# Performance work log

Measured on AMD Instinct MI355X. Metric: run time of the kernel, lower is better.

## Reference

```python
import jax, jax.numpy as jnp
import numpy as np

N = 1024        # hidden_size
M = 16000       # output_size (vocab)
T = 50          # encoder sequence length
NP = 50         # max_length (attention proj dim n_prime)


def setup_inputs() -> dict:
    key = jax.random.key(0)
    ks = jax.random.split(key, 24)
    f32 = jnp.float32
    def rnd(k, shape):
        return jax.random.normal(k, shape, dtype=f32) * 0.02
    inp = {
        'output': jax.random.normal(ks[0], (M, 1), dtype=f32),
        'hidden': jax.random.normal(ks[1], (N, 1), dtype=f32),
        'encoder_outputs': jax.random.normal(ks[2], (T, 2 * N), dtype=f32),
        # decoder GRU-like weights
        'W':  rnd(ks[3], (M, N)),
        'Wz': rnd(ks[4], (M, N)),
        'Wr': rnd(ks[5], (M, N)),
        'Wo': rnd(ks[6], (M, 2 * N)),
        'U':  rnd(ks[7], (N, N)),
        'Uz': rnd(ks[8], (N, N)),
        'Ur': rnd(ks[9], (N, N)),
        'Uo': rnd(ks[10], (4 * N, N)),
        'C':  rnd(ks[11], (2 * N, N)),
        'Cz': rnd(ks[12], (2 * N, N)),
        'Cr': rnd(ks[13], (2 * N, N)),
        'Co': rnd(ks[14], (4 * N, 2 * N)),
        'Vo': rnd(ks[15], (4 * N, M)),
        # attention weights
        'Va': rnd(ks[16], (NP, 1)),
        'Wa': rnd(ks[17], (NP, N)),
        'Ua': rnd(ks[18], (NP, 2 * N)),
    }
    return inp


def reference(output, hidden, encoder_outputs, W, Wz, Wr, Wo, U, Uz, Ur, Uo,
              C, Cz, Cr, Co, Vo, Va, Wa, Ua):
    y, s, h = output, hidden, encoder_outputs  # (M,1), (N,1), (T,2N)
    # --- Bahdanau attention (vectorized version of get_c's python loop) ---
    # e_i = exp(Va^T tanh(Wa@s + Ua@h_i)); then normalized -> softmax
    scores = jnp.tanh((Wa @ s).T + h @ Ua.T) @ Va          # (T,1)
    attn = jax.nn.softmax(scores[:, 0])                     # (T,)
    alpha = h * attn[:, None]                               # (T,2N) weighted enc outputs
    c = jnp.sum(alpha, axis=0)[:, None]                     # (2N,1) context
    # --- GRU-like decoder step (note: s_tilde uses sigmoid, per source) ---
    r = jax.nn.sigmoid(Wr.T @ y + Ur.T @ s + Cr.T @ c)      # (N,1)
    z = jax.nn.sigmoid(Wz.T @ y + Uz.T @ s + Cz.T @ c)      # (N,1)
    s_tilde = jax.nn.sigmoid(W.T @ y + U.T @ (r * s) + C.T @ c)
    s_new = (1.0 - z) * s + z * s_tilde                     # (N,1)
    # --- maxout output layer ---
    t_tilde = jax.nn.sigmoid(Uo @ s_new + Vo @ y + Co @ c)  # (4N,1)
    t = jnp.max(t_tilde.reshape(-1, 2, 1), axis=1)          # (2N,1) pairwise max
    logits = Wo @ t                                         # (M,1)
    log_sm = jax.nn.log_softmax(logits, axis=0)             # log(softmax(., dim=0))
    # dropout in the source is applied to a discarded value -> mathematical no-op
    return (log_sm, s_new, alpha)
```

## Files before the change

kernel.cpp:

```cpp
#include <hip/hip_runtime.h>
#include <math.h>

#define DEV_INLINE __device__ __forceinline__

DEV_INLINE float sigmoidf_(float x) { return 1.0f / (1.0f + expf(-x)); }

DEV_INLINE void colgemv_block(const float* __restrict__ A, const float* __restrict__ x,
                              float* __restrict__ out, int r0, int r1) {
    int c4 = threadIdx.x;
    const float4* A4 = (const float4*)A;
    float4 acc = make_float4(0.f, 0.f, 0.f, 0.f);
    for (int r = r0; r < r1; ++r) {
        float xv = x[r];
        float4 a = A4[(size_t)r * 256 + c4];
        acc.x = fmaf(xv, a.x, acc.x);
        acc.y = fmaf(xv, a.y, acc.y);
        acc.z = fmaf(xv, a.z, acc.z);
        acc.w = fmaf(xv, a.w, acc.w);
    }
    int c = c4 * 4;
    atomicAdd(out + c + 0, acc.x);
    atomicAdd(out + c + 1, acc.y);
    atomicAdd(out + c + 2, acc.z);
    atomicAdd(out + c + 3, acc.w);
}

DEV_INLINE float wave_dot(const float* __restrict__ row, const float* __restrict__ x,
                          int nv, int lane) {
    const float4* r4 = (const float4*)row;
    const float4* x4 = (const float4*)x;
    float acc = 0.f;
    for (int i = lane; i < nv; i += 64) {
        float4 a = r4[i], b = x4[i];
        acc = fmaf(a.x, b.x, fmaf(a.y, b.y, fmaf(a.z, b.z, fmaf(a.w, b.w, acc))));
    }
#pragma unroll
    for (int off = 32; off; off >>= 1) acc += __shfl_down(acc, off, 64);
    return acc;
}

__global__ void k_phaseA(const float* __restrict__ W, const float* __restrict__ Wz,
                         const float* __restrict__ Wr, const float* __restrict__ Uz,
                         const float* __restrict__ Ur, const float* __restrict__ Vo,
                         const float* __restrict__ Wa, const float* __restrict__ y,
                         const float* __restrict__ s, float* acc_r, float* acc_z,
                         float* acc_st, float* acc_t, float* ws50) {
    int b = blockIdx.x;
    if (b < 128) { colgemv_block(W, y, acc_st, b * 125, b * 125 + 125); return; }
    b -= 128;
    if (b < 128) { colgemv_block(Wz, y, acc_z, b * 125, b * 125 + 125); return; }
    b -= 128;
    if (b < 128) { colgemv_block(Wr, y, acc_r, b * 125, b * 125 + 125); return; }
    b -= 128;
    if (b < 8) { colgemv_block(Uz, s, acc_z, b * 128, b * 128 + 128); return; }
    b -= 8;
    if (b < 8) { colgemv_block(Ur, s, acc_r, b * 128, b * 128 + 128); return; }
    b -= 8;
    if (b < 1024) {
        int wid = (b * 256 + threadIdx.x) >> 6;
        int lane = threadIdx.x & 63;
        float v = wave_dot(Vo + (size_t)wid * 16000, y, 4000, lane);
        if (lane == 0) acc_t[wid] = v;
        return;
    }
    b -= 1024;
    {
        int wid = (b * 256 + threadIdx.x) >> 6;
        int lane = threadIdx.x & 63;
        if (wid < 50) {
            float v = wave_dot(Wa + wid * 1024, s, 256, lane);
            if (lane == 0) ws50[wid] = v;
        }
    }
}

__global__ void k_escore(const float* __restrict__ h, const float* __restrict__ Ua,
                         const float* __restrict__ ws50, float* __restrict__ em) {
    int wid = (blockIdx.x * blockDim.x + threadIdx.x) >> 6;
    int lane = threadIdx.x & 63;
    if (wid >= 2500) return;
    int i = wid / 50, j = wid - i * 50;
    float d = wave_dot(h + i * 2048, Ua + j * 2048, 512, lane);
    if (lane == 0) em[wid] = tanhf(ws50[j] + d);
}

__global__ void k_alpha_c(const float* __restrict__ h, const float* __restrict__ Va,
                          const float* __restrict__ em, float* __restrict__ cvec,
                          float* __restrict__ alpha_out) {
    __shared__ float attn_s[50];
    int tid = threadIdx.x;
    if (tid < 64) {
        float sc = -1e30f;
        if (tid < 50) {
            float t = 0.f;
            for (int j = 0; j < 50; ++j) t = fmaf(Va[j], em[tid * 50 + j], t);
            sc = t;
        }
        float m = sc;
#pragma unroll
        for (int off = 32; off; off >>= 1) m = fmaxf(m, __shfl_xor(m, off, 64));
        float e = (tid < 50) ? expf(sc - m) : 0.f;
        float ssum = e;
#pragma unroll
        for (int off = 32; off; off >>= 1) ssum += __shfl_xor(ssum, off, 64);
        if (tid < 50) attn_s[tid] = e / ssum;
    }
    __syncthreads();
    int g = blockIdx.x * 256 + tid;
    float csum = 0.f;
    for (int i = 0; i < 50; ++i) {
        float a = h[i * 2048 + g] * attn_s[i];
        alpha_out[i * 2048 + g] = a;
        csum += a;
    }
    cvec[g] = csum;
}

__global__ void k_phaseB(const float* __restrict__ C, const float* __restrict__ Cz,
                         const float* __restrict__ Cr, const float* __restrict__ cvec,
                         float* acc_st, float* acc_z, float* acc_r) {
    int b = blockIdx.x;
    if (b < 16) { colgemv_block(C, cvec, acc_st, b * 128, b * 128 + 128); return; }
    b -= 16;
    if (b < 16) { colgemv_block(Cz, cvec, acc_z, b * 128, b * 128 + 128); return; }
    b -= 16;
    colgemv_block(Cr, cvec, acc_r, b * 128, b * 128 + 128);
}

__global__ void k_rz(const float* __restrict__ acc_r, const float* __restrict__ acc_z,
                     const float* __restrict__ s, float* __restrict__ rs,
                     float* __restrict__ zbuf) {
    int n = blockIdx.x * 256 + threadIdx.x;
    float r = sigmoidf_(acc_r[n]);
    zbuf[n] = sigmoidf_(acc_z[n]);
    rs[n] = r * s[n];
}

__global__ void k_Ust(const float* __restrict__ U, const float* __restrict__ rs,
                      float* acc_st) {
    int b = blockIdx.x;
    colgemv_block(U, rs, acc_st, b * 128, b * 128 + 128);
}

__global__ void k_snew(const float* __restrict__ acc_st, const float* __restrict__ zbuf,
                       const float* __restrict__ s, float* __restrict__ snew,
                       float* __restrict__ out_snew) {
    int n = blockIdx.x * 256 + threadIdx.x;
    float st = sigmoidf_(acc_st[n]);
    float z = zbuf[n];
    float v = (1.f - z) * s[n] + z * st;
    snew[n] = v;
    out_snew[n] = v;
}

__global__ void k_uoco(const float* __restrict__ Uo, const float* __restrict__ Co,
                       const float* __restrict__ snew, const float* __restrict__ cvec,
                       float* __restrict__ acc_t) {
    int wid = (blockIdx.x * 256 + threadIdx.x) >> 6;
    int lane = threadIdx.x & 63;
    float d1 = wave_dot(Uo + (size_t)wid * 1024, snew, 256, lane);
    float d2 = wave_dot(Co + (size_t)wid * 2048, cvec, 512, lane);
    if (lane == 0) acc_t[wid] += d1 + d2;
}

__global__ void k_tmax(const float* __restrict__ acc_t, float* __restrict__ tvec) {
    int k = blockIdx.x * 256 + threadIdx.x;
    tvec[k] = fmaxf(sigmoidf_(acc_t[2 * k]), sigmoidf_(acc_t[2 * k + 1]));
}

__global__ void k_wo(const float* __restrict__ Wo, const float* __restrict__ tvec,
                     float* __restrict__ logits) {
    int wid = (blockIdx.x * 256 + threadIdx.x) >> 6;
    int lane = threadIdx.x & 63;
    float v = wave_dot(Wo + (size_t)wid * 2048, tvec, 512, lane);
    if (lane == 0) logits[wid] = v;
}

__global__ void k_logsm(float* __restrict__ out) {
    __shared__ float red[16];
    __shared__ float bval;
    int tid = threadIdx.x, lane = tid & 63, w = tid >> 6;
    float m = -1e30f;
    for (int i = tid; i < 16000; i += 1024) m = fmaxf(m, out[i]);
#pragma unroll
    for (int off = 32; off; off >>= 1) m = fmaxf(m, __shfl_xor(m, off, 64));
    if (lane == 0) red[w] = m;
    __syncthreads();
    if (tid == 0) {
        float mm = red[0];
        for (int i = 1; i < 16; ++i) mm = fmaxf(mm, red[i]);
        bval = mm;
    }
    __syncthreads();
    float M = bval;
    float sum = 0.f;
    for (int i = tid; i < 16000; i += 1024) sum += expf(out[i] - M);
#pragma unroll
    for (int off = 32; off; off >>= 1) sum += __shfl_xor(sum, off, 64);
    if (lane == 0) red[w] = sum;
    __syncthreads();
    if (tid == 0) {
        float ss = 0.f;
        for (int i = 0; i < 16; ++i) ss += red[i];
        bval = M + logf(ss);
    }
    __syncthreads();
    float lse = bval;
    for (int i = tid; i < 16000; i += 1024) out[i] -= lse;
}

extern "C" void kernel_launch(void* const* d_in, const int* in_sizes, int n_in,
                              void* d_out, int out_size, void* d_ws, size_t ws_size,
                              hipStream_t stream) {
    const float* y  = (const float*)d_in[0];
    const float* s  = (const float*)d_in[1];
    const float* h  = (const float*)d_in[2];
    const float* W  = (const float*)d_in[3];
    const float* Wz = (const float*)d_in[4];
    const float* Wr = (const float*)d_in[5];
    const float* Wo = (const float*)d_in[6];
    const float* U  = (const float*)d_in[7];
    const float* Uz = (const float*)d_in[8];
    const float* Ur = (const float*)d_in[9];
    const float* Uo = (const float*)d_in[10];
    const float* C  = (const float*)d_in[11];
    const float* Cz = (const float*)d_in[12];
    const float* Cr = (const float*)d_in[13];
    const float* Co = (const float*)d_in[14];
    const float* Vo = (const float*)d_in[15];
    const float* Va = (const float*)d_in[16];
    const float* Wa = (const float*)d_in[17];
    const float* Ua = (const float*)d_in[18];

    float* out = (float*)d_out;
    float* ws  = (float*)d_ws;

    float* acc_r  = ws;
    float* acc_z  = ws + 1024;
    float* acc_st = ws + 2048;
    float* acc_t  = ws + 3072;
    float* ws50   = ws + 7168;
    float* em     = ws + 7232;
    float* cvec   = ws + 9792;
    float* rs     = ws + 11840;
    float* zbuf   = ws + 12864;
    float* snew   = ws + 13888;
    float* tvec   = ws + 14912;

    hipMemsetAsync(ws, 0, 7168 * sizeof(float), stream);
    k_phaseA<<<1437, 256, 0, stream>>>(W, Wz, Wr, Uz, Ur, Vo, Wa, y, s,
                                       acc_r, acc_z, acc_st, acc_t, ws50);
    k_escore<<<625, 256, 0, stream>>>(h, Ua, ws50, em);
    k_alpha_c<<<8, 256, 0, stream>>>(h, Va, em, cvec, out + 17024);
    k_phaseB<<<48, 256, 0, stream>>>(C, Cz, Cr, cvec, acc_st, acc_z, acc_r);
    k_rz<<<4, 256, 0, stream>>>(acc_r, acc_z, s, rs, zbuf);
    k_Ust<<<8, 256, 0, stream>>>(U, rs, acc_st);
    k_snew<<<4, 256, 0, stream>>>(acc_st, zbuf, s, snew, out + 16000);
    k_uoco<<<1024, 256, 0, stream>>>(Uo, Co, snew, cvec, acc_t);
    k_tmax<<<8, 256, 0, stream>>>(acc_t, tvec);
    k_wo<<<4000, 256, 0, stream>>>(Wo, tvec, out);
    k_logsm<<<1, 1024, 0, stream>>>(out);
}
```

Measured before the change: 690.9 us.

## Reorder pipeline: attention first, fuse gate GEMVs and elementwise steps into fewer kernels

Attention scores are now computed first in a single kernel that merges the Wa and Ua dot products. The large y-driven GEMVs (W, Wz, Wr, Vo) are moved into one big kernel after the context vector, together with the C/Cz/Cr and Co products. The r/z, U, s_new and Uo steps are fused into two kernels that recompute small vectors in shared memory, which cuts the launch count and removes intermediate buffers. The dot-product and column-GEMV loops gain multiple accumulators and unrolled loads for more memory-level parallelism. The trade-off is that the attention step now sits serially in front of the big weight stream, with no overlap, and each k_uoco_snew block redundantly recomputes s_new.

```diff
diff --git a/kernel.cpp b/kernel.cpp
--- a/kernel.cpp
+++ b/kernel.cpp
@@ -4,84 +4,86 @@
 #define DEV_INLINE __device__ __forceinline__
 
 DEV_INLINE float sigmoidf_(float x) { return 1.0f / (1.0f + expf(-x)); }
+
+DEV_INLINE float wave_reduce(float v) {
+#pragma unroll
+    for (int off = 32; off; off >>= 1) v += __shfl_down(v, off, 64);
+    return v;
+}
+
+DEV_INLINE float wave_dotN(const float* __restrict__ row, const float* __restrict__ x,
+                           int nv, int lane) {
+    const float4* r4 = (const float4*)row;
+    const float4* x4 = (const float4*)x;
+    float a0 = 0.f, a1 = 0.f, a2 = 0.f, a3 = 0.f;
+    int i = lane;
+    for (; i + 192 < nv; i += 256) {
+        float4 p0 = r4[i],       q0 = x4[i];
+        float4 p1 = r4[i + 64],  q1 = x4[i + 64];
+        float4 p2 = r4[i + 128], q2 = x4[i + 128];
+        float4 p3 = r4[i + 192], q3 = x4[i + 192];
+        a0 = fmaf(p0.x, q0.x, fmaf(p0.y, q0.y, fmaf(p0.z, q0.z, fmaf(p0.w, q0.w, a0))));
+        a1 = fmaf(p1.x, q1.x, fmaf(p1.y, q1.y, fmaf(p1.z, q1.z, fmaf(p1.w, q1.w, a1))));
+        a2 = fmaf(p2.x, q2.x, fmaf(p2.y, q2.y, fmaf(p2.z, q2.z, fmaf(p2.w, q2.w, a2))));
+        a3 = fmaf(p3.x, q3.x, fmaf(p3.y, q3.y, fmaf(p3.z, q3.z, fmaf(p3.w, q3.w, a3))));
+    }
+    for (; i < nv; i += 64) {
+        float4 p = r4[i], q = x4[i];
+        a0 = fmaf(p.x, q.x, fmaf(p.y, q.y, fmaf(p.z, q.z, fmaf(p.w, q.w, a0))));
+    }
+    return wave_reduce(a0 + a1 + a2 + a3);
+}
 
 DEV_INLINE void colgemv_block(const float* __restrict__ A, const float* __restrict__ x,
                               float* __restrict__ out, int r0, int r1) {
     int c4 = threadIdx.x;
     const float4* A4 = (const float4*)A;
-    float4 acc = make_float4(0.f, 0.f, 0.f, 0.f);
-    for (int r = r0; r < r1; ++r) {
+    float4 s0 = make_float4(0.f, 0.f, 0.f, 0.f);
+    float4 s1 = make_float4(0.f, 0.f, 0.f, 0.f);
+    int r = r0;
+    for (; r + 8 <= r1; r += 8) {
+        float4 av[8];
+        float xs[8];
+#pragma unroll
+        for (int k = 0; k < 8; ++k) av[k] = A4[(size_t)(r + k) * 256 + c4];
+#pragma unroll
+        for (int k = 0; k < 8; ++k) xs[k] = x[r + k];
+#pragma unroll
+        for (int k = 0; k < 8; ++k) {
+            float4 a = av[k];
+            float xv = xs[k];
+            if (k & 1) {
+                s1.x = fmaf(xv, a.x, s1.x); s1.y = fmaf(xv, a.y, s1.y);
+                s1.z = fmaf(xv, a.z, s1.z); s1.w = fmaf(xv, a.w, s1.w);
+            } else {
+                s0.x = fmaf(xv, a.x, s0.x); s0.y = fmaf(xv, a.y, s0.y);
+                s0.z = fmaf(xv, a.z, s0.z); s0.w = fmaf(xv, a.w, s0.w);
+            }
+        }
+    }
+    for (; r < r1; ++r) {
         float xv = x[r];
         float4 a = A4[(size_t)r * 256 + c4];
-        acc.x = fmaf(xv, a.x, acc.x);
-        acc.y = fmaf(xv, a.y, acc.y);
-        acc.z = fmaf(xv, a.z, acc.z);
-        acc.w = fmaf(xv, a.w, acc.w);
+        s0.x = fmaf(xv, a.x, s0.x); s0.y = fmaf(xv, a.y, s0.y);
+        s0.z = fmaf(xv, a.z, s0.z); s0.w = fmaf(xv, a.w, s0.w);
     }
     int c = c4 * 4;
-    atomicAdd(out + c + 0, acc.x);
-    atomicAdd(out + c + 1, acc.y);
-    atomicAdd(out + c + 2, acc.z);
-    atomicAdd(out + c + 3, acc.w);
-}
-
-DEV_INLINE float wave_dot(const float* __restrict__ row, const float* __restrict__ x,
-                          int nv, int lane) {
-    const float4* r4 = (const float4*)row;
-    const float4* x4 = (const float4*)x;
-    float acc = 0.f;
-    for (int i = lane; i < nv; i += 64) {
-        float4 a = r4[i], b = x4[i];
-        acc = fmaf(a.x, b.x, fmaf(a.y, b.y, fmaf(a.z, b.z, fmaf(a.w, b.w, acc))));
-    }
-#pragma unroll
-    for (int off = 32; off; off >>= 1) acc += __shfl_down(acc, off, 64);
-    return acc;
-}
-
-__global__ void k_phaseA(const float* __restrict__ W, const float* __restrict__ Wz,
-                         const float* __restrict__ Wr, const float* __restrict__ Uz,
-                         const float* __restrict__ Ur, const float* __restrict__ Vo,
-                         const float* __restrict__ Wa, const float* __restrict__ y,
-                         const float* __restrict__ s, float* acc_r, float* acc_z,
-                         float* acc_st, float* acc_t, float* ws50) {
-    int b = blockIdx.x;
-    if (b < 128) { colgemv_block(W, y, acc_st, b * 125, b * 125 + 125); return; }
-    b -= 128;
-    if (b < 128) { colgemv_block(Wz, y, acc_z, b * 125, b * 125 + 125); return; }
-    b -= 128;
-    if (b < 128) { colgemv_block(Wr, y, acc_r, b * 125, b * 125 + 125); return; }
-    b -= 128;
-    if (b < 8) { colgemv_block(Uz, s, acc_z, b * 128, b * 128 + 128); return; }
-    b -= 8;
-    if (b < 8) { colgemv_block(Ur, s, acc_r, b * 128, b * 128 + 128); return; }
-    b -= 8;
-    if (b < 1024) {
-        int wid = (b * 256 + threadIdx.x) >> 6;
-        int lane = threadIdx.x & 63;
-        float v = wave_dot(Vo + (size_t)wid * 16000, y, 4000, lane);
-        if (lane == 0) acc_t[wid] = v;
-        return;
-    }
-    b -= 1024;
-    {
-        int wid = (b * 256 + threadIdx.x) >> 6;
-        int lane = threadIdx.x & 63;
-        if (wid < 50) {
-            float v = wave_dot(Wa + wid * 1024, s, 256, lane);
-            if (lane == 0) ws50[wid] = v;
-        }
-    }
-}
-
-__global__ void k_escore(const float* __restrict__ h, const float* __restrict__ Ua,
-                         const float* __restrict__ ws50, float* __restrict__ em) {
-    int wid = (blockIdx.x * blockDim.x + threadIdx.x) >> 6;
-    int lane = threadIdx.x & 63;
-    if (wid >= 2500) return;
-    int i = wid / 50, j = wid - i * 50;
-    float d = wave_dot(h + i * 2048, Ua + j * 2048, 512, lane);
-    if (lane == 0) em[wid] = tanhf(ws50[j] + d);
+    atomicAdd(out + c + 0, s0.x + s1.x);
+    atomicAdd(out + c + 1, s0.y + s1.y);
+    atomicAdd(out + c + 2, s0.z + s1.z);
+    atomicAdd(out + c + 3, s0.w + s1.w);
+}
+
+__global__ void k_scores(const float* __restrict__ Wa, const float* __restrict__ Ua,
+                         const float* __restrict__ h, const float* __restrict__ s,
+                         float* __restrict__ em) {
+    int i = blockIdx.x;
+    int w = threadIdx.x >> 6, lane = threadIdx.x & 63;
+    for (int j = w; j < 50; j += 4) {
+        float d1 = wave_dotN(Wa + j * 1024, s, 256, lane);
+        float d2 = wave_dotN(Ua + j * 2048, h + i * 2048, 512, lane);
+        if (lane == 0) em[i * 50 + j] = tanhf(d1 + d2);
+    }
 }
 
 __global__ void k_alpha_c(const float* __restrict__ h, const float* __restrict__ Va,
@@ -116,51 +118,75 @@
     cvec[g] = csum;
 }
 
-__global__ void k_phaseB(const float* __restrict__ C, const float* __restrict__ Cz,
-                         const float* __restrict__ Cr, const float* __restrict__ cvec,
-                         float* acc_st, float* acc_z, float* acc_r) {
+__global__ void k_megaA(const float* __restrict__ W, const float* __restrict__ Wz,
+                        const float* __restrict__ Wr, const float* __restrict__ Uz,
+                        const float* __restrict__ Ur, const float* __restrict__ C,
+                        const float* __restrict__ Cz, const float* __restrict__ Cr,
+                        const float* __restrict__ Vo, const float* __restrict__ Co,
+                        const float* __restrict__ y, const float* __restrict__ s,
+                        const float* __restrict__ cvec, float* acc_r, float* acc_z,
+                        float* acc_st, float* acc_t) {
     int b = blockIdx.x;
+    if (b < 128) { colgemv_block(W, y, acc_st, b * 125, b * 125 + 125); return; }
+    b -= 128;
+    if (b < 128) { colgemv_block(Wz, y, acc_z, b * 125, b * 125 + 125); return; }
+    b -= 128;
+    if (b < 128) { colgemv_block(Wr, y, acc_r, b * 125, b * 125 + 125); return; }
+    b -= 128;
+    if (b < 8) { colgemv_block(Uz, s, acc_z, b * 128, b * 128 + 128); return; }
+    b -= 8;
+    if (b < 8) { colgemv_block(Ur, s, acc_r, b * 128, b * 128 + 128); return; }
+    b -= 8;
     if (b < 16) { colgemv_block(C, cvec, acc_st, b * 128, b * 128 + 128); return; }
     b -= 16;
     if (b < 16) { colgemv_block(Cz, cvec, acc_z, b * 128, b * 128 + 128); return; }
     b -= 16;
-    colgemv_block(Cr, cvec, acc_r, b * 128, b * 128 + 128);
-}
-
-__global__ void k_rz(const float* __restrict__ acc_r, const float* __restrict__ acc_z,
-                     const float* __restrict__ s, float* __restrict__ rs,
-                     float* __restrict__ zbuf) {
-    int n = blockIdx.x * 256 + threadIdx.x;
-    float r = sigmoidf_(acc_r[n]);
-    zbuf[n] = sigmoidf_(acc_z[n]);
-    rs[n] = r * s[n];
-}
-
-__global__ void k_Ust(const float* __restrict__ U, const float* __restrict__ rs,
-                      float* acc_st) {
-    int b = blockIdx.x;
-    colgemv_block(U, rs, acc_st, b * 128, b * 128 + 128);
-}
-
-__global__ void k_snew(const float* __restrict__ acc_st, const float* __restrict__ zbuf,
-                       const float* __restrict__ s, float* __restrict__ snew,
-                       float* __restrict__ out_snew) {
-    int n = blockIdx.x * 256 + threadIdx.x;
-    float st = sigmoidf_(acc_st[n]);
-    float z = zbuf[n];
-    float v = (1.f - z) * s[n] + z * st;
-    snew[n] = v;
-    out_snew[n] = v;
-}
-
-__global__ void k_uoco(const float* __restrict__ Uo, const float* __restrict__ Co,
-                       const float* __restrict__ snew, const float* __restrict__ cvec,
-                       float* __restrict__ acc_t) {
-    int wid = (blockIdx.x * 256 + threadIdx.x) >> 6;
-    int lane = threadIdx.x & 63;
-    float d1 = wave_dot(Uo + (size_t)wid * 1024, snew, 256, lane);
-    float d2 = wave_dot(Co + (size_t)wid * 2048, cvec, 512, lane);
-    if (lane == 0) acc_t[wid] += d1 + d2;
+    if (b < 16) { colgemv_block(Cr, cvec, acc_r, b * 128, b * 128 + 128); return; }
+    b -= 16;
+    {
+        int wid = (b * 256 + threadIdx.x) >> 6;
+        int lane = threadIdx.x & 63;
+        float v1 = wave_dotN(Vo + (size_t)wid * 16000, y, 4000, lane);
+        float v2 = wave_dotN(Co + (size_t)wid * 2048, cvec, 512, lane);
+        if (lane == 0) acc_t[wid] = v1 + v2;
+    }
+}
+
+__global__ void k_rzUst(const float* __restrict__ U, const float* __restrict__ acc_r,
+                        const float* __restrict__ s, float* acc_st) {
+    __shared__ float rs_s[1024];
+    int tid = threadIdx.x;
+#pragma unroll
+    for (int k = 0; k < 4; ++k) {
+        int n = tid + 256 * k;
+        rs_s[n] = sigmoidf_(acc_r[n]) * s[n];
+    }
+    __syncthreads();
+    colgemv_block(U, rs_s, acc_st, blockIdx.x * 128, blockIdx.x * 128 + 128);
+}
+
+__global__ void k_uoco_snew(const float* __restrict__ Uo, const float* __restrict__ acc_st,
+                            const float* __restrict__ acc_z, const float* __restrict__ s,
+                            float* __restrict__ acc_t, float* __restrict__ out_snew) {
+    __shared__ float sn[1024];
+    int tid = threadIdx.x;
+#pragma unroll
+    for (int k = 0; k < 4; ++k) {
+        int n = tid + 256 * k;
+        float z = sigmoidf_(acc_z[n]);
+        float st = sigmoidf_(acc_st[n]);
+        float v = (1.f - z) * s[n] + z * st;
+        sn[n] = v;
+        if (blockIdx.x == 0) out_snew[n] = v;
+    }
+    __syncthreads();
+    int w = tid >> 6, lane = tid & 63;
+#pragma unroll
+    for (int k = 0; k < 4; ++k) {
+        int row = blockIdx.x * 16 + w * 4 + k;
+        float d = wave_dotN(Uo + (size_t)row * 1024, sn, 256, lane);
+        if (lane == 0) acc_t[row] += d;
+    }
 }
 
 __global__ void k_tmax(const float* __restrict__ acc_t, float* __restrict__ tvec) {
@@ -172,7 +198,7 @@
                      float* __restrict__ logits) {
     int wid = (blockIdx.x * 256 + threadIdx.x) >> 6;
     int lane = threadIdx.x & 63;
-    float v = wave_dot(Wo + (size_t)wid * 2048, tvec, 512, lane);
+    float v = wave_dotN(Wo + (size_t)wid * 2048, tvec, 512, lane);
     if (lane == 0) logits[wid] = v;
 }
 
@@ -239,24 +265,17 @@
     float* acc_z  = ws + 1024;
     float* acc_st = ws + 2048;
     float* acc_t  = ws + 3072;
-    float* ws50   = ws + 7168;
-    float* em     = ws + 7232;
-    float* cvec   = ws + 9792;
-    float* rs     = ws + 11840;
-    float* zbuf   = ws + 12864;
-    float* snew   = ws + 13888;
-    float* tvec   = ws + 14912;
-
-    hipMemsetAsync(ws, 0, 7168 * sizeof(float), stream);
-    k_phaseA<<<1437, 256, 0, stream>>>(W, Wz, Wr, Uz, Ur, Vo, Wa, y, s,
-                                       acc_r, acc_z, acc_st, acc_t, ws50);
-    k_escore<<<625, 256, 0, stream>>>(h, Ua, ws50, em);
+    float* em     = ws + 7168;
+    float* cvec   = ws + 9728;
+    float* tvec   = ws + 11776;
+
+    hipMemsetAsync(ws, 0, 3072 * sizeof(float), stream);
+    k_scores<<<50, 256, 0, stream>>>(Wa, Ua, h, s, em);
     k_alpha_c<<<8, 256, 0, stream>>>(h, Va, em, cvec, out + 17024);
-    k_phaseB<<<48, 256, 0, stream>>>(C, Cz, Cr, cvec, acc_st, acc_z, acc_r);
-    k_rz<<<4, 256, 0, stream>>>(acc_r, acc_z, s, rs, zbuf);
-    k_Ust<<<8, 256, 0, stream>>>(U, rs, acc_st);
-    k_snew<<<4, 256, 0, stream>>>(acc_st, zbuf, s, snew, out + 16000);
-    k_uoco<<<1024, 256, 0, stream>>>(Uo, Co, snew, cvec, acc_t);
+    k_megaA<<<1472, 256, 0, stream>>>(W, Wz, Wr, Uz, Ur, C, Cz, Cr, Vo, Co,
+                                      y, s, cvec, acc_r, acc_z, acc_st, acc_t);
+    k_rzUst<<<8, 256, 0, stream>>>(U, acc_r, s, acc_st);
+    k_uoco_snew<<<256, 256, 0, stream>>>(Uo, acc_st, acc_z, s, acc_t, out + 16000);
     k_tmax<<<8, 256, 0, stream>>>(acc_t, tvec);
     k_wo<<<4000, 256, 0, stream>>>(Wo, tvec, out);
     k_logsm<<<1, 1024, 0, stream>>>(out);
```

Result: no change. 682.3 us (-1.2%).
